# Optimization experiments

Hardware: AMD Instinct MI355X
Metric: run time of the kernel (lower is better)

## Reference

```python
import jax, jax.numpy as jnp
import numpy as np
import math

B, CK, T, H, W = 4, 64, 8, 30, 54
N, CV = 8, 512

def setup_inputs() -> dict:
    key = jax.random.key(0)
    k1, k2, k3, k4 = jax.random.split(key, 4)
    mem_keys = jax.random.normal(k1, (B, CK, T, H, W), dtype=jnp.float32)
    mem_values = jax.random.normal(k2, (N, CV, T, H, W), dtype=jnp.float32)
    qk = jax.random.normal(k3, (B, CK, H, W), dtype=jnp.float32)
    broadcast_map = jax.random.randint(k4, (N,), 0, B, dtype=jnp.int64)
    return {"mem_keys": mem_keys, "mem_values": mem_values, "qk": qk,
            "broadcast_map": broadcast_map}

def reference(mem_keys, mem_values, qk, broadcast_map):
    # STCNModel.read_memory
    Bq, CKq, Tq, Hq, Wq = mem_keys.shape
    mk = mem_keys.reshape(Bq, CKq, Tq * Hq * Wq)      # [B, CK, THW]
    q = qk.reshape(Bq, CKq, Hq * Wq)                   # [B, CK, HW]
    a_sq = jnp.sum(mk * mk, axis=1)[:, :, None]        # [B, THW, 1]
    ab = jnp.einsum('bct,bcq->btq', mk, q)             # [B, THW, HW]
    frame_affinity = (2.0 * ab - a_sq) / math.sqrt(CKq)
    # softmax over memory dim (axis=1)
    frame_affinity = jax.nn.softmax(frame_affinity, axis=1)
    obj_affinity = frame_affinity[broadcast_map]       # [N, THW, HW]
    Nn, CVv = mem_values.shape[0], mem_values.shape[1]
    mo = mem_values.reshape(Nn, CVv, Tq * Hq * Wq)     # [N, CV, THW]
    obj_read = jnp.einsum('nct,ntq->ncq', mo, obj_affinity)
    return obj_read.reshape(Nn, CVv, Hq, Wq)
```

## Files before the change

### kernel.cpp

```cpp
#include <hip/hip_runtime.h>
#include <hip/hip_bf16.h>

#define CKDIM 64
#define THW   12960
#define HWDIM 1620
#define NOBJ  8
#define CVAL  512
#define NB    4
#define NSTEP 405
#define NJT   13
#define NJT2  7
#define NCHS  8
#define NCHP  4
#define PCH   16
#define S2F   0.3606737602222409f

#if defined(__has_builtin)
#if __has_builtin(__builtin_amdgcn_global_load_lds)
#define HAVE_GLL 1
#endif
#endif

using bf16x8 = __attribute__((ext_vector_type(8))) short;
using f32x4  = __attribute__((ext_vector_type(4))) float;

__device__ __forceinline__ unsigned cvtpk(float lo, float hi) {
    unsigned r;
    asm("v_cvt_pk_bf16_f32 %0, %1, %2" : "=v"(r) : "v"(lo), "v"(hi));
    return r;
}
__device__ __forceinline__ unsigned short bf_rne(float x) {
    unsigned u = __float_as_uint(x);
    u += 0x7FFFu + ((u >> 16) & 1u);
    return (unsigned short)(u >> 16);
}
__device__ __forceinline__ float fexp2(float x) {
#if __has_builtin(__builtin_amdgcn_exp2f)
    return __builtin_amdgcn_exp2f(x);
#else
    return __expf(x * 0.69314718055994531f);
#endif
}
#ifdef HAVE_GLL
__device__ __forceinline__ void gload16(const void* g, void* l) {
    __builtin_amdgcn_global_load_lds(
        (const __attribute__((address_space(1))) unsigned int*)g,
        (__attribute__((address_space(3))) unsigned int*)l, 16, 0, 0);
}
#endif

__global__ void stcn_ksq_kernel(const float* __restrict__ mk, float* __restrict__ k8l) {
    int t = blockIdx.x * 256 + threadIdx.x;
    if (t >= THW) return;
    int b = blockIdx.y;
    const float* p = mk + (size_t)b * CKDIM * THW + t;
    float s = 0.f;
#pragma unroll
    for (int c = 0; c < CKDIM; ++c) { float v = p[(size_t)c * THW]; s = fmaf(v, v, s); }
    k8l[b * THW + t] = s * (0.125f * 1.44269504088896341f);
}

__global__ __launch_bounds__(512)
void stcn_ktr_kernel(const float* __restrict__ mk, unsigned short* __restrict__ kbt,
                     float* __restrict__ k8l) {
    __shared__ unsigned short L[64][72];
    __shared__ float S[64][8];
    const int tid = threadIdx.x, b = blockIdx.y, t0 = blockIdx.x * 64;
    const int tt = tid & 63;
    float a2 = 0.f;
#pragma unroll
    for (int it = 0; it < 8; ++it) {
        int idx = tid + 512 * it;
        int c = idx >> 6;
        int t = t0 + tt;
        float v = (t < THW) ? mk[((size_t)b * CKDIM + c) * THW + t] : 0.f;
        L[tt][c] = bf_rne(v);
        a2 = fmaf(v, v, a2);
    }
    S[tt][tid >> 6] = a2;
    __syncthreads();
    if (tid < 64) {
        float s = 0.f;
#pragma unroll
        for (int q = 0; q < 8; ++q) s += S[tid][q];
        int t = t0 + tid;
        if (t < THW) k8l[b * THW + t] = s * (0.125f * 1.44269504088896341f);
    }
    {
        int tr = tid >> 3, cq = tid & 7;
        int t = t0 + tr;
        if (t < THW) {
            uint4 o = *(const uint4*)&L[tr][8 * cq];
            *(uint4*)(kbt + ((size_t)b * THW + t) * CKDIM + 8 * cq) = o;
        }
    }
}

__global__ void stcn_vcvt_kernel(const float* __restrict__ mv, unsigned short* __restrict__ mvb) {
    size_t i = ((size_t)blockIdx.x * 256 + threadIdx.x) * 8;
    if (i >= (size_t)NOBJ * CVAL * THW) return;
    float4 v0 = *(const float4*)(mv + i);
    float4 v1 = *(const float4*)(mv + i + 4);
    uint4 o;
    o.x = cvtpk(v0.x, v0.y); o.y = cvtpk(v0.z, v0.w);
    o.z = cvtpk(v1.x, v1.y); o.w = cvtpk(v1.z, v1.w);
    *(uint4*)(mvb + i) = o;
}

template <int MODE, bool VB16, bool KB16>
__global__ __launch_bounds__(512, (MODE == 1) ? 4 : 1)
void stcn_aff_kernel(const float* __restrict__ mk, const unsigned short* __restrict__ kbt,
                     const float* __restrict__ qk, const float* __restrict__ k8l,
                     float* __restrict__ mpart, float* __restrict__ lpart,
                     const float* __restrict__ mv, const unsigned short* __restrict__ mvb,
                     const int* __restrict__ bmap, float* __restrict__ out)
{
    constexpr int SMEM_BYTES = (MODE == 0) ? 36864 : 45312;
    __shared__ __align__(16) unsigned char smem[SMEM_BYTES];
    unsigned short* KtP   = (unsigned short*)smem;
    float*          k8tP  = (float*)(smem + 9216);
    unsigned short* PtP   = (unsigned short*)(smem + 9472);
    unsigned short* VtP   = (unsigned short*)(smem + 23808);
    float*          mjsP  = (float*)(smem + 44288);
    float*          iljsP = (float*)(smem + 44800);
    unsigned short* QtP   = (unsigned short*)smem;

    const int tid  = threadIdx.x;
    const int w    = tid >> 6;
    const int lane = tid & 63;
    const int g    = lane >> 4;
    const int lr   = lane & 15;

    int b, n = 0, jt, kc, cb = 0;
    if (MODE == 0) { b = blockIdx.y; jt = blockIdx.x >> 3; kc = blockIdx.x & 7; }
    else {
        n = blockIdx.y; jt = blockIdx.x >> 3; kc = (blockIdx.x >> 1) & 3; cb = blockIdx.x & 1;
        b = bmap[n];
    }
    const int jbase = jt * 128;
    const int cbase = cb * 256;

#pragma unroll
    for (int it = 0; it < 8; ++it) {
        int idx = tid + 512 * it;
        int j = idx & 127, cp = idx >> 7;
        int jg = jbase + j;
        float q0 = 0.f, q1 = 0.f;
        if (jg < HWDIM) {
            const float* qp = qk + ((size_t)b * CKDIM + 2 * cp) * HWDIM + jg;
            q0 = qp[0]; q1 = qp[HWDIM];
        }
        unsigned wh = cvtpk(q0, q1);
        float r0 = q0 - __uint_as_float(wh << 16);
        float r1 = q1 - __uint_as_float(wh & 0xFFFF0000u);
        *(unsigned*)&QtP[(0 * 128 + j) * 72 + 2 * cp] = wh;
        *(unsigned*)&QtP[(1 * 128 + j) * 72 + 2 * cp] = cvtpk(r0, r1);
    }
    __syncthreads();
    bf16x8 bqh[2], bql[2];
#pragma unroll
    for (int s = 0; s < 2; ++s) {
        bqh[s] = *(const bf16x8*)&QtP[(0 * 128 + w * 16 + lr) * 72 + 32 * s + 8 * g];
        bql[s] = *(const bf16x8*)&QtP[(1 * 128 + w * 16 + lr) * 72 + 32 * s + 8 * g];
    }
    __syncthreads();

    auto stageK_loads = [&](int st, uint2& k16, float2* kvf) {
        if constexpr (KB16) {
            int tt = tid >> 4, cq = tid & 15;
            k16 = *(const uint2*)(kbt + ((size_t)b * THW + st * 32 + tt) * CKDIM + 4 * cq);
        } else {
#pragma unroll
            for (int it = 0; it < 2; ++it) {
                int idx = tid + 512 * it;
                int tt = idx & 31, cp = idx >> 5;
                const float* kp = mk + ((size_t)b * CKDIM + 2 * cp) * THW + st * 32 + tt;
                kvf[it].x = kp[0];
                kvf[it].y = kp[THW];
            }
        }
    };
    auto stageK_write = [&](int buf, uint2 k16, const float2* kvf) {
        if constexpr (KB16) {
            int tt = tid >> 4, cq = tid & 15;
            *(uint2*)&KtP[(buf * 32 + tt) * 72 + 4 * cq] = k16;
        } else {
#pragma unroll
            for (int it = 0; it < 2; ++it) {
                int idx = tid + 512 * it;
                int tt = idx & 31, cp = idx >> 5;
                *(unsigned*)&KtP[(buf * 32 + tt) * 72 + 2 * cp] = cvtpk(kvf[it].x, kvf[it].y);
            }
        }
    };

    int s0, s1;
    if (MODE == 0) { s0 = (NSTEP * kc) / NCHS; s1 = (NSTEP * (kc + 1)) / NCHS; }
    else           { s0 = (NSTEP * kc) / NCHP; s1 = (NSTEP * (kc + 1)) / NCHP; }

    if (MODE == 1 && tid < 128) {
        int jg = jbase + tid;
        float m = 0.f, l = 0.f;
        if (jg < HWDIM) {
            m = -1e30f;
#pragma unroll
            for (int c = 0; c < NCHS; ++c) {
                float mc = mpart[(b * NCHS + c) * HWDIM + jg];
                float lc = lpart[(b * NCHS + c) * HWDIM + jg];
                float mn = fmaxf(m, mc);
                l = l * fexp2(m - mn) + lc * fexp2(mc - mn);
                m = mn;
            }
        }
        mjsP[tid]  = m;
        iljsP[tid] = (l > 0.f) ? 1.f / l : 0.f;
    }
    {
        uint2 k16; float2 kvf[2];
        stageK_loads(s0, k16, kvf);
        stageK_write(0, k16, kvf);
        if (tid < 32) k8tP[tid] = k8l[b * THW + s0 * 32 + tid];
    }
    __syncthreads();

    float mv_j = 0.f, il_j = 0.f;
    if (MODE == 1) { mv_j = mjsP[w * 16 + lr]; il_j = iljsP[w * 16 + lr]; }

    float m_run = -1e30f, l_run = 0.f;
    f32x4 zz = {0.f, 0.f, 0.f, 0.f};
    f32x4 acc[4][4];
    if (MODE == 1)
#pragma unroll
        for (int i = 0; i < 4; ++i)
#pragma unroll
            for (int j = 0; j < 4; ++j) acc[i][j] = zz;

    const int wc = w >> 1, wj = w & 1;
    const int vc = tid >> 1, vth = tid & 1;

    int cur = 0;
    for (int st = s0; st < s1; ++st) {
        const int t0 = st * 32;
        const bool nxt = (st + 1 < s1);

        uint4 vw0 = {0,0,0,0}, vw1 = {0,0,0,0};
        if (MODE == 1) {
            if (VB16) {
                const unsigned short* vp = mvb + ((size_t)n * CVAL + cbase + vc) * THW + t0 + vth * 16;
                vw0 = *(const uint4*)vp;
                vw1 = *(const uint4*)(vp + 8);
            } else {
                const float* vp = mv + ((size_t)n * CVAL + cbase + vc) * THW + t0 + vth * 16;
                float4 f0 = *(const float4*)vp;
                float4 f1 = *(const float4*)(vp + 4);
                float4 f2 = *(const float4*)(vp + 8);
                float4 f3 = *(const float4*)(vp + 12);
                vw0 = make_uint4(cvtpk(f0.x,f0.y), cvtpk(f0.z,f0.w), cvtpk(f1.x,f1.y), cvtpk(f1.z,f1.w));
                vw1 = make_uint4(cvtpk(f2.x,f2.y), cvtpk(f2.z,f2.w), cvtpk(f3.x,f3.y), cvtpk(f3.z,f3.w));
            }
        }
        uint2 k16; float2 kvf[2];
        float k8next = 0.f;
        if (nxt) {
            stageK_loads(st + 1, k16, kvf);
            if (tid < 32) k8next = k8l[b * THW + (st + 1) * 32 + tid];
        }
        bf16x8 ak0[2], ak1[2];
#pragma unroll
        for (int s = 0; s < 2; ++s) {
            ak0[s] = *(const bf16x8*)&KtP[(cur * 32 + lr) * 72 + 32 * s + 8 * g];
            ak1[s] = *(const bf16x8*)&KtP[(cur * 32 + 16 + lr) * 72 + 32 * s + 8 * g];
        }
        f32x4 k80 = *(const f32x4*)&k8tP[cur * 32 + 4 * g];
        f32x4 k81 = *(const f32x4*)&k8tP[cur * 32 + 16 + 4 * g];
        f32x4 ab0 = zz, ab1 = zz;
#pragma unroll
        for (int s = 0; s < 2; ++s) {
            ab0 = __builtin_amdgcn_mfma_f32_16x16x32_bf16(ak0[s], bqh[s], ab0, 0, 0, 0);
            ab0 = __builtin_amdgcn_mfma_f32_16x16x32_bf16(ak0[s], bql[s], ab0, 0, 0, 0);
            ab1 = __builtin_amdgcn_mfma_f32_16x16x32_bf16(ak1[s], bqh[s], ab1, 0, 0, 0);
            ab1 = __builtin_amdgcn_mfma_f32_16x16x32_bf16(ak1[s], bql[s], ab1, 0, 0, 0);
        }
        if (nxt) {
            stageK_write(cur ^ 1, k16, kvf);
            if (tid < 32) k8tP[(cur ^ 1) * 32 + tid] = k8next;
        }

        if (MODE == 0) {
            float L0[4], L1[4], tmax = -1e30f;
#pragma unroll
            for (int r = 0; r < 4; ++r) {
                L0[r] = fmaf(ab0[r], S2F, -k80[r]); tmax = fmaxf(tmax, L0[r]);
                L1[r] = fmaf(ab1[r], S2F, -k81[r]); tmax = fmaxf(tmax, L1[r]);
            }
            float ps = 0.f;
#pragma unroll
            for (int r = 0; r < 4; ++r)
                ps += fexp2(L0[r] - tmax) + fexp2(L1[r] - tmax);
            float mn = fmaxf(m_run, tmax);
            l_run = l_run * fexp2(m_run - mn) + ps * fexp2(tmax - mn);
            m_run = mn;
            __syncthreads();
        } else {
            float p0[4], p1[4];
#pragma unroll
            for (int r = 0; r < 4; ++r) {
                p0[r] = fexp2(fmaf(ab0[r], S2F, -k80[r]) - mv_j) * il_j;
                p1[r] = fexp2(fmaf(ab1[r], S2F, -k81[r]) - mv_j) * il_j;
            }
            __syncthreads();
            {
                int jl = w * 16 + lr;
                *(uint2*)&PtP[jl * 56 + 4 * g]      = make_uint2(cvtpk(p0[0], p0[1]), cvtpk(p0[2], p0[3]));
                *(uint2*)&PtP[jl * 56 + 16 + 4 * g] = make_uint2(cvtpk(p1[0], p1[1]), cvtpk(p1[2], p1[3]));
                *(uint4*)&VtP[vc * 40 + vth * 16]     = vw0;
                *(uint4*)&VtP[vc * 40 + vth * 16 + 8] = vw1;
            }
            __syncthreads();
            bf16x8 bp[4];
#pragma unroll
            for (int jf = 0; jf < 4; ++jf)
                bp[jf] = *(const bf16x8*)&PtP[(wj * 64 + jf * 16 + lr) * 56 + 8 * g];
#pragma unroll
            for (int cf = 0; cf < 4; ++cf) {
                bf16x8 av = *(const bf16x8*)&VtP[(wc * 64 + cf * 16 + lr) * 40 + 8 * g];
#pragma unroll
                for (int jf = 0; jf < 4; ++jf)
                    acc[cf][jf] = __builtin_amdgcn_mfma_f32_16x16x32_bf16(av, bp[jf], acc[cf][jf], 0, 0, 0);
            }
        }
        cur ^= 1;
    }

    if (MODE == 0) {
#pragma unroll
        for (int off = 16; off < 64; off <<= 1) {
            float mo = __shfl_xor(m_run, off, 64);
            float lo = __shfl_xor(l_run, off, 64);
            float mn = fmaxf(m_run, mo);
            l_run = l_run * fexp2(m_run - mn) + lo * fexp2(mo - mn);
            m_run = mn;
        }
        int jg = jbase + w * 16 + lr;
        if (g == 0 && jg < HWDIM) {
            mpart[(b * NCHS + kc) * HWDIM + jg] = m_run;
            lpart[(b * NCHS + kc) * HWDIM + jg] = l_run;
        }
    } else {
#pragma unroll
        for (int cf = 0; cf < 4; ++cf) {
#pragma unroll
            for (int jf = 0; jf < 4; ++jf) {
                int jg = jbase + wj * 64 + jf * 16 + lr;
                if (jg < HWDIM) {
                    int c = cbase + wc * 64 + cf * 16 + 4 * g;
                    float* op = out + ((size_t)n * CVAL + c) * HWDIM + jg;
#pragma unroll
                    for (int r = 0; r < 4; ++r)
                        atomicAdd(op + (size_t)r * HWDIM, acc[cf][jf][r]);
                }
            }
        }
    }
}

__global__ __launch_bounds__(512)
void stcn_pwrite_kernel(const unsigned short* __restrict__ kbt,
                        const float* __restrict__ qk, const float* __restrict__ k8l,
                        const float* __restrict__ mpart, const float* __restrict__ lpart,
                        unsigned short* __restrict__ Pws, int bbase)
{
    __shared__ __align__(16) unsigned char smem[36864];
    unsigned short* KtP   = (unsigned short*)smem;
    float*          k8tP  = (float*)(smem + 9216);
    unsigned short* PtP   = (unsigned short*)(smem + 9472);
    float*          mjsP  = (float*)(smem + 23808);
    float*          iljsP = (float*)(smem + 24320);
    unsigned short* QtP   = (unsigned short*)smem;

    const int tid  = threadIdx.x;
    const int w    = tid >> 6;
    const int lane = tid & 63;
    const int g    = lane >> 4;
    const int lr   = lane & 15;

    const int bb = blockIdx.y;
    const int b  = bbase + bb;
    const int jt = blockIdx.x >> 4, kc = blockIdx.x & 15;
    const int jbase = jt * 128;

#pragma unroll
    for (int it = 0; it < 8; ++it) {
        int idx = tid + 512 * it;
        int j = idx & 127, cp = idx >> 7;
        int jg = jbase + j;
        float q0 = 0.f, q1 = 0.f;
        if (jg < HWDIM) {
            const float* qp = qk + ((size_t)b * CKDIM + 2 * cp) * HWDIM + jg;
            q0 = qp[0]; q1 = qp[HWDIM];
        }
        unsigned wh = cvtpk(q0, q1);
        float r0 = q0 - __uint_as_float(wh << 16);
        float r1 = q1 - __uint_as_float(wh & 0xFFFF0000u);
        *(unsigned*)&QtP[(0 * 128 + j) * 72 + 2 * cp] = wh;
        *(unsigned*)&QtP[(1 * 128 + j) * 72 + 2 * cp] = cvtpk(r0, r1);
    }
    __syncthreads();
    bf16x8 bqh[2], bql[2];
#pragma unroll
    for (int s = 0; s < 2; ++s) {
        bqh[s] = *(const bf16x8*)&QtP[(0 * 128 + w * 16 + lr) * 72 + 32 * s + 8 * g];
        bql[s] = *(const bf16x8*)&QtP[(1 * 128 + w * 16 + lr) * 72 + 32 * s + 8 * g];
    }
    __syncthreads();

    const int s0 = (NSTEP * kc) / PCH, s1 = (NSTEP * (kc + 1)) / PCH;

    if (tid < 128) {
        int jg = jbase + tid;
        float m = 0.f, l = 0.f;
        if (jg < HWDIM) {
            m = -1e30f;
#pragma unroll
            for (int c = 0; c < NCHS; ++c) {
                float mc = mpart[(b * NCHS + c) * HWDIM + jg];
                float lc = lpart[(b * NCHS + c) * HWDIM + jg];
                float mn = fmaxf(m, mc);
                l = l * fexp2(m - mn) + lc * fexp2(mc - mn);
                m = mn;
            }
        }
        mjsP[tid]  = m;
        iljsP[tid] = (l > 0.f) ? 1.f / l : 0.f;
    }
    {
        int tt = tid >> 4, cq = tid & 15;
        uint2 k16 = *(const uint2*)(kbt + ((size_t)b * THW + s0 * 32 + tt) * CKDIM + 4 * cq);
        *(uint2*)&KtP[tt * 72 + 4 * cq] = k16;
        if (tid < 32) k8tP[tid] = k8l[b * THW + s0 * 32 + tid];
    }
    __syncthreads();

    const float mv_j = mjsP[w * 16 + lr], il_j = iljsP[w * 16 + lr];
    f32x4 zz = {0.f, 0.f, 0.f, 0.f};

    int cur = 0;
    for (int st = s0; st < s1; ++st) {
        const int t0 = st * 32;
        const bool nxt = (st + 1 < s1);
        uint2 k16;
        float k8next = 0.f;
        const int tt = tid >> 4, cq = tid & 15;
        if (nxt) {
            k16 = *(const uint2*)(kbt + ((size_t)b * THW + (st + 1) * 32 + tt) * CKDIM + 4 * cq);
            if (tid < 32) k8next = k8l[b * THW + (st + 1) * 32 + tid];
        }
        bf16x8 ak0[2], ak1[2];
#pragma unroll
        for (int s = 0; s < 2; ++s) {
            ak0[s] = *(const bf16x8*)&KtP[(cur * 32 + lr) * 72 + 32 * s + 8 * g];
            ak1[s] = *(const bf16x8*)&KtP[(cur * 32 + 16 + lr) * 72 + 32 * s + 8 * g];
        }
        f32x4 k80 = *(const f32x4*)&k8tP[cur * 32 + 4 * g];
        f32x4 k81 = *(const f32x4*)&k8tP[cur * 32 + 16 + 4 * g];
        f32x4 ab0 = zz, ab1 = zz;
#pragma unroll
        for (int s = 0; s < 2; ++s) {
            ab0 = __builtin_amdgcn_mfma_f32_16x16x32_bf16(ak0[s], bqh[s], ab0, 0, 0, 0);
            ab0 = __builtin_amdgcn_mfma_f32_16x16x32_bf16(ak0[s], bql[s], ab0, 0, 0, 0);
            ab1 = __builtin_amdgcn_mfma_f32_16x16x32_bf16(ak1[s], bqh[s], ab1, 0, 0, 0);
            ab1 = __builtin_amdgcn_mfma_f32_16x16x32_bf16(ak1[s], bql[s], ab1, 0, 0, 0);
        }
        if (nxt) {
            *(uint2*)&KtP[((cur ^ 1) * 32 + tt) * 72 + 4 * cq] = k16;
            if (tid < 32) k8tP[(cur ^ 1) * 32 + tid] = k8next;
        }
        float p0[4], p1[4];
#pragma unroll
        for (int r = 0; r < 4; ++r) {
            p0[r] = fexp2(fmaf(ab0[r], S2F, -k80[r]) - mv_j) * il_j;
            p1[r] = fexp2(fmaf(ab1[r], S2F, -k81[r]) - mv_j) * il_j;
        }
        __syncthreads();
        {
            int jl = w * 16 + lr;
            *(uint2*)&PtP[jl * 56 + 4 * g]      = make_uint2(cvtpk(p0[0], p0[1]), cvtpk(p0[2], p0[3]));
            *(uint2*)&PtP[jl * 56 + 16 + 4 * g] = make_uint2(cvtpk(p1[0], p1[1]), cvtpk(p1[2], p1[3]));
        }
        __syncthreads();
        {
            int jr = tid >> 2, qq = tid & 3;
            int jg = jbase + jr;
            if (jg < HWDIM)
                *(uint4*)(Pws + ((size_t)bb * HWDIM + jg) * THW + t0 + qq * 8) =
                    *(const uint4*)&PtP[jr * 56 + qq * 8];
        }
        cur ^= 1;
    }
}

__global__ __launch_bounds__(1024, 4)
void stcn_gemm4_kernel(const unsigned short* __restrict__ mvb,
                       const unsigned short* __restrict__ Pws,
                       const int* __restrict__ bmap, float* __restrict__ out)
{
    __shared__ __align__(16) unsigned short Av[2][256 * 32];
    __shared__ __align__(16) unsigned short Bv[2][256 * 32];

    const int wg  = blockIdx.x;
    const int vid = (wg & 7) * 56 + (wg >> 3);
    const int n   = vid / 56;
    const int r   = vid % 56;
    const int cm  = r / 28;
    const int r2  = r % 28;
    const int ks  = r2 / 7;
    const int jn  = r2 % 7;
    const int b = bmap[n];
    const int jbase = jn * 256, cbase = cm * 256;

    const int tid = threadIdx.x;
    const int w = tid >> 6, lane = tid & 63, g = lane >> 4, lr = lane & 15;
    const int wc = w >> 2, wj = w & 3;

    const int srow = tid >> 2;
    const int tsw  = (((tid & 3) ^ ((tid >> 3) & 3)) << 3);
    const int gs8  = ((g ^ ((lr >> 1) & 3)) << 3);

    const int s0 = (NSTEP * ks) / 4, s1 = (NSTEP * (ks + 1)) / 4;

    const unsigned short* ga = mvb + ((size_t)n * CVAL + cbase + srow) * THW + tsw;
    int jr = jbase + srow; if (jr >= HWDIM) jr = 0;
    const unsigned short* gb = Pws + ((size_t)b * HWDIM + jr) * THW + tsw;

    f32x4 zz = {0.f, 0.f, 0.f, 0.f};
    f32x4 acc[4][4];
#pragma unroll
    for (int i = 0; i < 4; ++i)
#pragma unroll
        for (int j = 0; j < 4; ++j) acc[i][j] = zz;

#ifdef HAVE_GLL
    auto stage = [&](int buf, int st) {
        const int t0 = st * 32;
        gload16(ga + t0, &Av[buf][w * 512]);
        gload16(gb + t0, &Bv[buf][w * 512]);
    };
    stage(0, s0);
#else
    {
        const int t0 = s0 * 32;
        *(uint4*)&Av[0][tid * 8] = *(const uint4*)(ga + t0);
        *(uint4*)&Bv[0][tid * 8] = *(const uint4*)(gb + t0);
    }
#endif
    __syncthreads();

    int cur = 0;
    for (int st = s0; st < s1; ++st) {
        const bool nxt = (st + 1 < s1);
#ifdef HAVE_GLL
        if (nxt) stage(cur ^ 1, st + 1);
#else
        uint4 ra, rb;
        if (nxt) {
            const int t0 = (st + 1) * 32;
            ra = *(const uint4*)(ga + t0);
            rb = *(const uint4*)(gb + t0);
        }
#endif
        bf16x8 av[4], bp[4];
#pragma unroll
        for (int cf = 0; cf < 4; ++cf)
            av[cf] = *(const bf16x8*)&Av[cur][(wc * 64 + cf * 16 + lr) * 32 + gs8];
#pragma unroll
        for (int jf = 0; jf < 4; ++jf)
            bp[jf] = *(const bf16x8*)&Bv[cur][(wj * 64 + jf * 16 + lr) * 32 + gs8];
#pragma unroll
        for (int cf = 0; cf < 4; ++cf)
#pragma unroll
            for (int jf = 0; jf < 4; ++jf)
                acc[cf][jf] = __builtin_amdgcn_mfma_f32_16x16x32_bf16(av[cf], bp[jf], acc[cf][jf], 0, 0, 0);
#ifndef HAVE_GLL
        if (nxt) {
            *(uint4*)&Av[cur ^ 1][tid * 8] = ra;
            *(uint4*)&Bv[cur ^ 1][tid * 8] = rb;
        }
#endif
        __syncthreads();
        cur ^= 1;
    }

#pragma unroll
    for (int cf = 0; cf < 4; ++cf)
#pragma unroll
        for (int jf = 0; jf < 4; ++jf) {
            int jg = jbase + wj * 64 + jf * 16 + lr;
            if (jg < HWDIM) {
                int c = cbase + wc * 64 + cf * 16 + 4 * g;
                float* op = out + ((size_t)n * CVAL + c) * HWDIM + jg;
#pragma unroll
                for (int r4 = 0; r4 < 4; ++r4)
                    atomicAdd(op + (size_t)r4 * HWDIM, acc[cf][jf][r4]);
            }
        }
}

__global__ __launch_bounds__(256, 4)
void stcn_gemm3_kernel(const unsigned short* __restrict__ mvb,
                       const unsigned short* __restrict__ Pws,
                       const int* __restrict__ bmap, float* __restrict__ out, int phase)
{
    __shared__ __align__(16) unsigned short Av[2][128 * 32];
    __shared__ __align__(16) unsigned short Bv[2][128 * 32];

    const int n = blockIdx.y;
    const int b = bmap[n];
    if ((b >> 1) != phase) return;
    const int bslot = b & 1;

    const int x = blockIdx.x;
    const int ks = x & 1;
    const int rest = x >> 1;
    const int jn = rest % NJT;
    const int cm = rest / NJT;
    const int jbase = jn * 128, cbase = cm * 128;

    const int tid = threadIdx.x;
    const int w = tid >> 6, lane = tid & 63, g = lane >> 4, lr = lane & 15;
    const int wc = w >> 1, wj = w & 1;

    const int srow = tid >> 2;
    const int tsw  = (((tid & 3) ^ ((tid >> 3) & 3)) << 3);
    const int gs8  = ((g ^ ((lr >> 1) & 3)) << 3);

    const int s0 = (NSTEP * ks) / 2, s1 = (NSTEP * (ks + 1)) / 2;

    const unsigned short* abase = mvb + ((size_t)n * CVAL + cbase) * THW;
    const unsigned short* bbase = Pws + (size_t)bslot * HWDIM * THW;
    int jr0 = jbase + srow;       if (jr0 >= HWDIM) jr0 = 0;
    int jr1 = jbase + 64 + srow;  if (jr1 >= HWDIM) jr1 = 0;
    const unsigned short* ga0 = abase + (size_t)(srow) * THW + tsw;
    const unsigned short* ga1 = abase + (size_t)(64 + srow) * THW + tsw;
    const unsigned short* gb0 = bbase + (size_t)jr0 * THW + tsw;
    const unsigned short* gb1 = bbase + (size_t)jr1 * THW + tsw;

    f32x4 zz = {0.f, 0.f, 0.f, 0.f};
    f32x4 acc[4][4];
#pragma unroll
    for (int i = 0; i < 4; ++i)
#pragma unroll
        for (int j = 0; j < 4; ++j) acc[i][j] = zz;

#ifdef HAVE_GLL
    auto stage = [&](int buf, int st) {
        const int t0 = st * 32;
        gload16(ga0 + t0, &Av[buf][0    + w * 512]);
        gload16(ga1 + t0, &Av[buf][2048 + w * 512]);
        gload16(gb0 + t0, &Bv[buf][0    + w * 512]);
        gload16(gb1 + t0, &Bv[buf][2048 + w * 512]);
    };
    stage(0, s0);
#else
    {
        const int t0 = s0 * 32;
        *(uint4*)&Av[0][tid * 8]        = *(const uint4*)(ga0 + t0);
        *(uint4*)&Av[0][2048 + tid * 8] = *(const uint4*)(ga1 + t0);
        *(uint4*)&Bv[0][tid * 8]        = *(const uint4*)(gb0 + t0);
        *(uint4*)&Bv[0][2048 + tid * 8] = *(const uint4*)(gb1 + t0);
    }
#endif
    __syncthreads();

    int cur = 0;
    for (int st = s0; st < s1; ++st) {
        const bool nxt = (st + 1 < s1);
#ifdef HAVE_GLL
        if (nxt) stage(cur ^ 1, st + 1);
#else
        uint4 ra0, ra1, rb0, rb1;
        if (nxt) {
            const int t0 = (st + 1) * 32;
            ra0 = *(const uint4*)(ga0 + t0);
            ra1 = *(const uint4*)(ga1 + t0);
            rb0 = *(const uint4*)(gb0 + t0);
            rb1 = *(const uint4*)(gb1 + t0);
        }
#endif
        bf16x8 av[4], bp[4];
#pragma unroll
        for (int cf = 0; cf < 4; ++cf)
            av[cf] = *(const bf16x8*)&Av[cur][(wc * 64 + cf * 16 + lr) * 32 + gs8];
#pragma unroll
        for (int jf = 0; jf < 4; ++jf)
            bp[jf] = *(const bf16x8*)&Bv[cur][(wj * 64 + jf * 16 + lr) * 32 + gs8];
#pragma unroll
        for (int cf = 0; cf < 4; ++cf)
#pragma unroll
            for (int jf = 0; jf < 4; ++jf)
                acc[cf][jf] = __builtin_amdgcn_mfma_f32_16x16x32_bf16(av[cf], bp[jf], acc[cf][jf], 0, 0, 0);
#ifndef HAVE_GLL
        if (nxt) {
            *(uint4*)&Av[cur ^ 1][tid * 8]        = ra0;
            *(uint4*)&Av[cur ^ 1][2048 + tid * 8] = ra1;
            *(uint4*)&Bv[cur ^ 1][tid * 8]        = rb0;
            *(uint4*)&Bv[cur ^ 1][2048 + tid * 8] = rb1;
        }
#endif
        __syncthreads();
        cur ^= 1;
    }

#pragma unroll
    for (int cf = 0; cf < 4; ++cf)
#pragma unroll
        for (int jf = 0; jf < 4; ++jf) {
            int jg = jbase + wj * 64 + jf * 16 + lr;
            if (jg < HWDIM) {
                int c = cbase + wc * 64 + cf * 16 + 4 * g;
                float* op = out + ((size_t)n * CVAL + c) * HWDIM + jg;
#pragma unroll
                for (int r4 = 0; r4 < 4; ++r4)
                    atomicAdd(op + (size_t)r4 * HWDIM, acc[cf][jf][r4]);
            }
        }
}

extern "C" void kernel_launch(void* const* d_in, const int* in_sizes, int n_in,
                              void* d_out, int out_size, void* d_ws, size_t ws_size,
                              hipStream_t stream) {
    (void)in_sizes; (void)n_in;
    const float* mk   = (const float*)d_in[0];
    const float* mv   = (const float*)d_in[1];
    const float* qkp  = (const float*)d_in[2];
    const int*   bmap = (const int*)d_in[3];
    float* out = (float*)d_out;

    float* k8l   = (float*)d_ws;
    float* mpart = k8l + NB * THW;
    float* lpart = mpart + NB * NCHS * HWDIM;
    unsigned short* mvb = (unsigned short*)(lpart + NB * NCHS * HWDIM);
    unsigned short* kbt = mvb + (size_t)NOBJ * CVAL * THW;
    unsigned short* Pws = kbt + (size_t)NB * THW * CKDIM;

    size_t base_bytes = (size_t)(NB * THW + 2 * NB * NCHS * HWDIM) * 4;
    size_t need_vb  = base_bytes + (size_t)NOBJ * CVAL * THW * 2;
    size_t need_kbt = need_vb + (size_t)NB * THW * CKDIM * 2;
    size_t need_P2  = need_kbt + (size_t)2 * HWDIM * THW * 2;
    size_t need_P4  = need_kbt + (size_t)4 * HWDIM * THW * 2;
    bool use_vb16 = (ws_size >= need_vb);
    bool use_kbt  = (ws_size >= need_kbt);
    bool use_P2   = (ws_size >= need_P2);
    bool use_P4   = (ws_size >= need_P4);

    hipMemsetAsync(d_out, 0, (size_t)out_size * sizeof(float), stream);
    if (use_kbt)
        stcn_ktr_kernel<<<dim3((THW + 63) / 64, NB), 512, 0, stream>>>(mk, kbt, k8l);
    else
        stcn_ksq_kernel<<<dim3((THW + 255) / 256, NB), 256, 0, stream>>>(mk, k8l);
    if (use_vb16) {
        size_t nthreads = (size_t)NOBJ * CVAL * THW / 8;
        stcn_vcvt_kernel<<<(unsigned)((nthreads + 255) / 256), 256, 0, stream>>>(mv, mvb);
    }

    if (use_kbt)
        stcn_aff_kernel<0, false, true><<<dim3(NJT * NCHS, NB), 512, 0, stream>>>(
            mk, kbt, qkp, k8l, mpart, lpart, nullptr, nullptr, nullptr, nullptr);
    else
        stcn_aff_kernel<0, false, false><<<dim3(NJT * NCHS, NB), 512, 0, stream>>>(
            mk, nullptr, qkp, k8l, mpart, lpart, nullptr, nullptr, nullptr, nullptr);

    if (use_P4 && use_kbt) {
        stcn_pwrite_kernel<<<dim3(NJT * PCH, NB), 512, 0, stream>>>(
            kbt, qkp, k8l, mpart, lpart, Pws, 0);
        stcn_gemm4_kernel<<<dim3(448), 1024, 0, stream>>>(mvb, Pws, bmap, out);
    } else if (use_P2 && use_kbt) {
        for (int p = 0; p < 2; ++p) {
            stcn_pwrite_kernel<<<dim3(NJT * PCH, 2), 512, 0, stream>>>(
                kbt, qkp, k8l, mpart, lpart, Pws, 2 * p);
            stcn_gemm3_kernel<<<dim3(104, NOBJ), 256, 0, stream>>>(
                mvb, Pws, bmap, out, p);
        }
    } else {
        dim3 g1(NJT * NCHP * 2, NOBJ);
        if (use_vb16 && use_kbt)
            stcn_aff_kernel<1, true, true><<<g1, 512, 0, stream>>>(
                mk, kbt, qkp, k8l, mpart, lpart, nullptr, mvb, bmap, out);
        else if (use_vb16)
            stcn_aff_kernel<1, true, false><<<g1, 512, 0, stream>>>(
                mk, nullptr, qkp, k8l, mpart, lpart, nullptr, mvb, bmap, out);
        else
            stcn_aff_kernel<1, false, false><<<g1, 512, 0, stream>>>(
                mk, nullptr, qkp, k8l, mpart, lpart, mv, nullptr, bmap, out);
    }
}
```

Before: 557.6 us.

## Replace gemm4 with 512-thread 256x256x64 phased MFMA GEMM over padded rows

Pads the bf16 value and probability row strides to THWP (a multiple of 64) and zero-fills the tail, so the K loop can use 64-wide chunks. The new GEMM uses 512 threads with 8x4 accumulator tiles per wave, a 64-wide K step, XOR-swizzled LDS, and four interleaved phases per step. Each phase overlaps staging of the next buffer with MFMA work using explicit vmcnt waits, barriers and setprio. It aims to raise MFMA density and cut the number of barrier-bound K steps, at the cost of higher register pressure, an extra padding kernel and more padded memory traffic.

```diff
diff --git a/kernel.cpp b/kernel.cpp
--- a/kernel.cpp
+++ b/kernel.cpp
@@ -3,13 +3,15 @@
 
 #define CKDIM 64
 #define THW   12960
+#define THWP  13056
+#define NKT   204
+#define KTCH  51
 #define HWDIM 1620
 #define NOBJ  8
 #define CVAL  512
 #define NB    4
 #define NSTEP 405
 #define NJT   13
-#define NJT2  7
 #define NCHS  8
 #define NCHP  4
 #define PCH   16
@@ -99,12 +101,25 @@
 __global__ void stcn_vcvt_kernel(const float* __restrict__ mv, unsigned short* __restrict__ mvb) {
     size_t i = ((size_t)blockIdx.x * 256 + threadIdx.x) * 8;
     if (i >= (size_t)NOBJ * CVAL * THW) return;
+    size_t row = i / THW, t = i % THW;
     float4 v0 = *(const float4*)(mv + i);
     float4 v1 = *(const float4*)(mv + i + 4);
     uint4 o;
     o.x = cvtpk(v0.x, v0.y); o.y = cvtpk(v0.z, v0.w);
     o.z = cvtpk(v1.x, v1.y); o.w = cvtpk(v1.z, v1.w);
-    *(uint4*)(mvb + i) = o;
+    *(uint4*)(mvb + row * THWP + t) = o;
+}
+
+__global__ void stcn_pad0_kernel(unsigned short* __restrict__ mvb,
+                                 unsigned short* __restrict__ Pws, int nPr) {
+    int idx = blockIdx.x * 256 + threadIdx.x;
+    int rowtot = NOBJ * CVAL + nPr;
+    if (idx >= rowtot * 12) return;
+    int row = idx / 12, ch = idx % 12;
+    unsigned short* base = (row < NOBJ * CVAL)
+        ? mvb + (size_t)row * THWP
+        : Pws + (size_t)(row - NOBJ * CVAL) * THWP;
+    *(uint4*)(base + THW + ch * 8) = make_uint4(0, 0, 0, 0);
 }
 
 template <int MODE, bool VB16, bool KB16>
@@ -246,7 +261,7 @@
         uint4 vw0 = {0,0,0,0}, vw1 = {0,0,0,0};
         if (MODE == 1) {
             if (VB16) {
-                const unsigned short* vp = mvb + ((size_t)n * CVAL + cbase + vc) * THW + t0 + vth * 16;
+                const unsigned short* vp = mvb + ((size_t)n * CVAL + cbase + vc) * THWP + t0 + vth * 16;
                 vw0 = *(const uint4*)vp;
                 vw1 = *(const uint4*)(vp + 8);
             } else {
@@ -492,118 +507,134 @@
             int jr = tid >> 2, qq = tid & 3;
             int jg = jbase + jr;
             if (jg < HWDIM)
-                *(uint4*)(Pws + ((size_t)bb * HWDIM + jg) * THW + t0 + qq * 8) =
+                *(uint4*)(Pws + ((size_t)bb * HWDIM + jg) * THWP + t0 + qq * 8) =
                     *(const uint4*)&PtP[jr * 56 + qq * 8];
         }
         cur ^= 1;
     }
 }
 
-__global__ __launch_bounds__(1024, 4)
-void stcn_gemm4_kernel(const unsigned short* __restrict__ mvb,
+#ifdef HAVE_GLL
+#define W4 asm volatile("s_waitcnt vmcnt(4)" ::: "memory")
+#define W2 asm volatile("s_waitcnt vmcnt(2)" ::: "memory")
+#define W0 asm volatile("s_waitcnt vmcnt(0)" ::: "memory")
+#define NOWAIT ((void)0)
+
+#define STAGE_A(H) { size_t o = ((size_t)((H)*128)) * THWP + (size_t)ktn * 64; \
+    gload16(sA + o, &Av[cn][(H)*8192 + w*512]); \
+    gload16(sA + o + (size_t)64 * THWP, &Av[cn][(H)*8192 + 4096 + w*512]); }
+#define STAGE_B(H) { \
+    gload16(sB[H][0] + (size_t)ktn * 64, &Bv[cn][(H)*8192 + w*512]); \
+    gload16(sB[H][1] + (size_t)ktn * 64, &Bv[cn][(H)*8192 + 4096 + w*512]); }
+
+#define PHASE(QM, QN, STAGE_STMT, WAIT_STMT) { \
+    bf16x8 av_[4][2], bp_[2][2]; \
+    _Pragma("unroll") for (int mf = 0; mf < 4; ++mf) \
+    _Pragma("unroll") for (int ksb = 0; ksb < 2; ++ksb) { \
+        int ra = wm*128 + ((QM)*4 + mf)*16 + lr; \
+        av_[mf][ksb] = *(const bf16x8*)&Av[bc][ra*64 + (((ksb*4 + g) ^ (ra & 7)) << 3)]; } \
+    _Pragma("unroll") for (int nf = 0; nf < 2; ++nf) \
+    _Pragma("unroll") for (int ksb = 0; ksb < 2; ++ksb) { \
+        int rb = wn*64 + ((QN)*2 + nf)*16 + lr; \
+        bp_[nf][ksb] = *(const bf16x8*)&Bv[bc][rb*64 + (((ksb*4 + g) ^ (rb & 7)) << 3)]; } \
+    STAGE_STMT; \
+    __builtin_amdgcn_s_barrier(); \
+    asm volatile("s_waitcnt lgkmcnt(0)" ::: "memory"); \
+    __builtin_amdgcn_sched_barrier(0); \
+    __builtin_amdgcn_s_setprio(1); \
+    _Pragma("unroll") for (int ksb = 0; ksb < 2; ++ksb) \
+    _Pragma("unroll") for (int mf = 0; mf < 4; ++mf) \
+    _Pragma("unroll") for (int nf = 0; nf < 2; ++nf) \
+        acc[(QM)*4 + mf][(QN)*2 + nf] = __builtin_amdgcn_mfma_f32_16x16x32_bf16( \
+            av_[mf][ksb], bp_[nf][ksb], acc[(QM)*4 + mf][(QN)*2 + nf], 0, 0, 0); \
+    __builtin_amdgcn_s_setprio(0); \
+    __builtin_amdgcn_sched_barrier(0); \
+    WAIT_STMT; \
+    __builtin_amdgcn_s_barrier(); \
+    __builtin_amdgcn_sched_barrier(0); }
+
+__global__ __launch_bounds__(512, 2)
+void stcn_gemm6_kernel(const unsigned short* __restrict__ mvb,
                        const unsigned short* __restrict__ Pws,
                        const int* __restrict__ bmap, float* __restrict__ out)
 {
-    __shared__ __align__(16) unsigned short Av[2][256 * 32];
-    __shared__ __align__(16) unsigned short Bv[2][256 * 32];
+    __shared__ __align__(16) unsigned short Av[2][256 * 64];
+    __shared__ __align__(16) unsigned short Bv[2][256 * 64];
 
     const int wg  = blockIdx.x;
     const int vid = (wg & 7) * 56 + (wg >> 3);
     const int n   = vid / 56;
-    const int r   = vid % 56;
-    const int cm  = r / 28;
-    const int r2  = r % 28;
-    const int ks  = r2 / 7;
-    const int jn  = r2 % 7;
+    int rr = vid % 56;
+    const int cm  = rr / 28; rr %= 28;
+    const int ks  = rr / 7;
+    const int jn  = rr % 7;
     const int b = bmap[n];
     const int jbase = jn * 256, cbase = cm * 256;
 
     const int tid = threadIdx.x;
     const int w = tid >> 6, lane = tid & 63, g = lane >> 4, lr = lane & 15;
-    const int wc = w >> 2, wj = w & 3;
-
-    const int srow = tid >> 2;
-    const int tsw  = (((tid & 3) ^ ((tid >> 3) & 3)) << 3);
-    const int gs8  = ((g ^ ((lr >> 1) & 3)) << 3);
-
-    const int s0 = (NSTEP * ks) / 4, s1 = (NSTEP * (ks + 1)) / 4;
-
-    const unsigned short* ga = mvb + ((size_t)n * CVAL + cbase + srow) * THW + tsw;
-    int jr = jbase + srow; if (jr >= HWDIM) jr = 0;
-    const unsigned short* gb = Pws + ((size_t)b * HWDIM + jr) * THW + tsw;
+    const int wm = w >> 2, wn = w & 3;
+
+    const int kt0 = ks * KTCH;
+
+    const int tsw = (((tid & 7) ^ ((tid >> 3) & 7)) << 3);
+    const unsigned short* sA = mvb + ((size_t)n * CVAL + cbase + (tid >> 3)) * THWP + tsw;
+    const unsigned short* sB[2][2];
+#pragma unroll
+    for (int h = 0; h < 2; ++h)
+#pragma unroll
+        for (int k = 0; k < 2; ++k) {
+            int jr = jbase + h * 128 + k * 64 + (tid >> 3);
+            if (jr >= HWDIM) jr = HWDIM - 1;
+            sB[h][k] = Pws + ((size_t)b * HWDIM + jr) * THWP + tsw;
+        }
 
     f32x4 zz = {0.f, 0.f, 0.f, 0.f};
-    f32x4 acc[4][4];
-#pragma unroll
-    for (int i = 0; i < 4; ++i)
+    f32x4 acc[8][4];
+#pragma unroll
+    for (int i = 0; i < 8; ++i)
 #pragma unroll
         for (int j = 0; j < 4; ++j) acc[i][j] = zz;
 
-#ifdef HAVE_GLL
-    auto stage = [&](int buf, int st) {
-        const int t0 = st * 32;
-        gload16(ga + t0, &Av[buf][w * 512]);
-        gload16(gb + t0, &Bv[buf][w * 512]);
-    };
-    stage(0, s0);
-#else
     {
-        const int t0 = s0 * 32;
-        *(uint4*)&Av[0][tid * 8] = *(const uint4*)(ga + t0);
-        *(uint4*)&Bv[0][tid * 8] = *(const uint4*)(gb + t0);
-    }
+        int cn = 0, ktn = kt0;
+        STAGE_A(0); STAGE_B(0); STAGE_A(1); STAGE_B(1);
+    }
+    W4;
+    __builtin_amdgcn_s_barrier();
+    __builtin_amdgcn_sched_barrier(0);
+
+    for (int i = 0; i < KTCH; ++i) {
+        const int bc = i & 1, cn = bc ^ 1;
+        const int ktn = kt0 + i + 1;
+        if (i + 1 < KTCH) {
+            PHASE(0, 0, STAGE_A(0), W4);
+            PHASE(1, 0, STAGE_B(0), W4);
+            PHASE(0, 1, STAGE_A(1), NOWAIT);
+            PHASE(1, 1, STAGE_B(1), W4);
+        } else {
+            PHASE(0, 0, NOWAIT, W2);
+            PHASE(1, 0, NOWAIT, W0);
+            PHASE(0, 1, NOWAIT, NOWAIT);
+            PHASE(1, 1, NOWAIT, NOWAIT);
+        }
+    }
+
+#pragma unroll
+    for (int mf = 0; mf < 8; ++mf)
+#pragma unroll
+        for (int nf = 0; nf < 4; ++nf) {
+            int jg = jbase + wn * 64 + nf * 16 + lr;
+            if (jg < HWDIM) {
+                int c = cbase + wm * 128 + mf * 16 + 4 * g;
+                float* op = out + ((size_t)n * CVAL + c) * HWDIM + jg;
+#pragma unroll
+                for (int r4 = 0; r4 < 4; ++r4)
+                    atomicAdd(op + (size_t)r4 * HWDIM, acc[mf][nf][r4]);
+            }
+        }
+}
 #endif
-    __syncthreads();
-
-    int cur = 0;
-    for (int st = s0; st < s1; ++st) {
-        const bool nxt = (st + 1 < s1);
-#ifdef HAVE_GLL
-        if (nxt) stage(cur ^ 1, st + 1);
-#else
-        uint4 ra, rb;
-        if (nxt) {
-            const int t0 = (st + 1) * 32;
-            ra = *(const uint4*)(ga + t0);
-            rb = *(const uint4*)(gb + t0);
-        }
-#endif
-        bf16x8 av[4], bp[4];
-#pragma unroll
-        for (int cf = 0; cf < 4; ++cf)
-            av[cf] = *(const bf16x8*)&Av[cur][(wc * 64 + cf * 16 + lr) * 32 + gs8];
-#pragma unroll
-        for (int jf = 0; jf < 4; ++jf)
-            bp[jf] = *(const bf16x8*)&Bv[cur][(wj * 64 + jf * 16 + lr) * 32 + gs8];
-#pragma unroll
-        for (int cf = 0; cf < 4; ++cf)
-#pragma unroll
-            for (int jf = 0; jf < 4; ++jf)
-                acc[cf][jf] = __builtin_amdgcn_mfma_f32_16x16x32_bf16(av[cf], bp[jf], acc[cf][jf], 0, 0, 0);
-#ifndef HAVE_GLL
-        if (nxt) {
-            *(uint4*)&Av[cur ^ 1][tid * 8] = ra;
-            *(uint4*)&Bv[cur ^ 1][tid * 8] = rb;
-        }
-#endif
-        __syncthreads();
-        cur ^= 1;
-    }
-
-#pragma unroll
-    for (int cf = 0; cf < 4; ++cf)
-#pragma unroll
-        for (int jf = 0; jf < 4; ++jf) {
-            int jg = jbase + wj * 64 + jf * 16 + lr;
-            if (jg < HWDIM) {
-                int c = cbase + wc * 64 + cf * 16 + 4 * g;
-                float* op = out + ((size_t)n * CVAL + c) * HWDIM + jg;
-#pragma unroll
-                for (int r4 = 0; r4 < 4; ++r4)
-                    atomicAdd(op + (size_t)r4 * HWDIM, acc[cf][jf][r4]);
-            }
-        }
-}
 
 __global__ __launch_bounds__(256, 4)
 void stcn_gemm3_kernel(const unsigned short* __restrict__ mvb,
@@ -635,14 +666,14 @@
 
     const int s0 = (NSTEP * ks) / 2, s1 = (NSTEP * (ks + 1)) / 2;
 
-    const unsigned short* abase = mvb + ((size_t)n * CVAL + cbase) * THW;
-    const unsigned short* bbase = Pws + (size_t)bslot * HWDIM * THW;
+    const unsigned short* abase = mvb + ((size_t)n * CVAL + cbase) * THWP;
+    const unsigned short* bbase = Pws + (size_t)bslot * HWDIM * THWP;
     int jr0 = jbase + srow;       if (jr0 >= HWDIM) jr0 = 0;
     int jr1 = jbase + 64 + srow;  if (jr1 >= HWDIM) jr1 = 0;
-    const unsigned short* ga0 = abase + (size_t)(srow) * THW + tsw;
-    const unsigned short* ga1 = abase + (size_t)(64 + srow) * THW + tsw;
-    const unsigned short* gb0 = bbase + (size_t)jr0 * THW + tsw;
-    const unsigned short* gb1 = bbase + (size_t)jr1 * THW + tsw;
+    const unsigned short* ga0 = abase + (size_t)(srow) * THWP + tsw;
+    const unsigned short* ga1 = abase + (size_t)(64 + srow) * THWP + tsw;
+    const unsigned short* gb0 = bbase + (size_t)jr0 * THWP + tsw;
+    const unsigned short* gb1 = bbase + (size_t)jr1 * THWP + tsw;
 
     f32x4 zz = {0.f, 0.f, 0.f, 0.f};
     f32x4 acc[4][4];
@@ -739,14 +770,14 @@
     float* mpart = k8l + NB * THW;
     float* lpart = mpart + NB * NCHS * HWDIM;
     unsigned short* mvb = (unsigned short*)(lpart + NB * NCHS * HWDIM);
-    unsigned short* kbt = mvb + (size_t)NOBJ * CVAL * THW;
+    unsigned short* kbt = mvb + (size_t)NOBJ * CVAL * THWP;
     unsigned short* Pws = kbt + (size_t)NB * THW * CKDIM;
 
     size_t base_bytes = (size_t)(NB * THW + 2 * NB * NCHS * HWDIM) * 4;
-    size_t need_vb  = base_bytes + (size_t)NOBJ * CVAL * THW * 2;
+    size_t need_vb  = base_bytes + (size_t)NOBJ * CVAL * THWP * 2;
     size_t need_kbt = need_vb + (size_t)NB * THW * CKDIM * 2;
-    size_t need_P2  = need_kbt + (size_t)2 * HWDIM * THW * 2;
-    size_t need_P4  = need_kbt + (size_t)4 * HWDIM * THW * 2;
+    size_t need_P2  = need_kbt + (size_t)2 * HWDIM * THWP * 2;
+    size_t need_P4  = need_kbt + (size_t)4 * HWDIM * THWP * 2;
     bool use_vb16 = (ws_size >= need_vb);
     bool use_kbt  = (ws_size >= need_kbt);
     bool use_P2   = (ws_size >= need_P2);
@@ -760,6 +791,9 @@
     if (use_vb16) {
         size_t nthreads = (size_t)NOBJ * CVAL * THW / 8;
         stcn_vcvt_kernel<<<(unsigned)((nthreads + 255) / 256), 256, 0, stream>>>(mv, mvb);
+        int nPr = use_P4 ? 4 * HWDIM : (use_P2 ? 2 * HWDIM : 0);
+        int nz = (NOBJ * CVAL + nPr) * 12;
+        stcn_pad0_kernel<<<(nz + 255) / 256, 256, 0, stream>>>(mvb, Pws, nPr);
     }
 
     if (use_kbt)
@@ -769,11 +803,14 @@
         stcn_aff_kernel<0, false, false><<<dim3(NJT * NCHS, NB), 512, 0, stream>>>(
             mk, nullptr, qkp, k8l, mpart, lpart, nullptr, nullptr, nullptr, nullptr);
 
+#ifdef HAVE_GLL
     if (use_P4 && use_kbt) {
         stcn_pwrite_kernel<<<dim3(NJT * PCH, NB), 512, 0, stream>>>(
             kbt, qkp, k8l, mpart, lpart, Pws, 0);
-        stcn_gemm4_kernel<<<dim3(448), 1024, 0, stream>>>(mvb, Pws, bmap, out);
-    } else if (use_P2 && use_kbt) {
+        stcn_gemm6_kernel<<<dim3(448), 512, 0, stream>>>(mvb, Pws, bmap, out);
+    } else
+#endif
+    if (use_P2 && use_kbt) {
         for (int p = 0; p < 2; ++p) {
             stcn_pwrite_kernel<<<dim3(NJT * PCH, 2), 512, 0, stream>>>(
                 kbt, qkp, k8l, mpart, lpart, Pws, 2 * p);
```

Result: slower. 590.0 us (+5.8%).
